# Optimization experiments

Hardware: AMD Instinct MI355X
Metric: run time of the kernel (lower is better)

## Reference

```python
import jax, jax.numpy as jnp
import numpy as np

EPS = 1e-5
GROUPS = 32

# 3x3 regular grid: row0 = dy, row1 = dx for kernel index k = ky*3 + kx
_REG = jnp.array([[-1, -1, -1, 0, 0, 0, 1, 1, 1],
                  [-1, 0, 1, -1, 0, 1, -1, 0, 1]], dtype=jnp.float32)


def conv2d(x, w, pad):
    return jax.lax.conv_general_dilated(
        x, w, window_strides=(1, 1), padding=((pad, pad), (pad, pad)),
        dimension_numbers=('NCHW', 'OIHW', 'NCHW'))


def deform_conv3x3(x, off_y, off_x, w_dcn, dilation):
    # x: (N,C,H,W); off_y/off_x: (N,H,W,9); w_dcn: (Cout,Cin,3,3)
    N, C, H, W = x.shape
    dyk = (jnp.arange(9) // 3 - 1).astype(jnp.float32) * dilation  # (9,)
    dxk = (jnp.arange(9) % 3 - 1).astype(jnp.float32) * dilation
    yy = jnp.arange(H, dtype=jnp.float32)
    xx = jnp.arange(W, dtype=jnp.float32)
    # sampling positions (padding == dilation, stride == 1)
    py = yy[None, :, None, None] + dyk[None, None, None, :] + off_y  # (N,H,W,9)
    px = xx[None, None, :, None] + dxk[None, None, None, :] + off_x

    y0 = jnp.floor(py)
    x0 = jnp.floor(px)
    wy1 = py - y0
    wx1 = px - x0

    xflat = x.reshape(N, C, H * W)

    def gather(xf, idx):  # xf (C,HW), idx (H,W,9) -> (C,H,W,9)
        return xf[:, idx]

    val = jnp.zeros((N, C, H, W, 9), dtype=x.dtype)
    corners = [
        (y0, x0, (1.0 - wy1) * (1.0 - wx1)),
        (y0, x0 + 1.0, (1.0 - wy1) * wx1),
        (y0 + 1.0, x0, wy1 * (1.0 - wx1)),
        (y0 + 1.0, x0 + 1.0, wy1 * wx1),
    ]
    for yc, xc, wc in corners:
        valid = ((yc >= 0) & (yc <= H - 1) & (xc >= 0) & (xc <= W - 1)).astype(x.dtype)
        yi = jnp.clip(yc, 0, H - 1).astype(jnp.int32)
        xi = jnp.clip(xc, 0, W - 1).astype(jnp.int32)
        ind = yi * W + xi  # (N,H,W,9)
        g = jax.vmap(gather)(xflat, ind)  # (N,C,H,W,9)
        val = val + g * (wc * valid)[:, None]

    Cout = w_dcn.shape[0]
    wk = w_dcn.reshape(Cout, C, 9)
    return jnp.einsum('nchwk,ock->nohw', val, wk)


def group_norm(x, gamma, beta, groups, eps):
    N, C, H, W = x.shape
    xg = x.reshape(N, groups, C // groups, H, W)
    mu = xg.mean(axis=(2, 3, 4), keepdims=True)
    var = xg.var(axis=(2, 3, 4), keepdims=True)
    xn = ((xg - mu) * jax.lax.rsqrt(var + eps)).reshape(N, C, H, W)
    return xn * gamma[None, :, None, None] + beta[None, :, None, None]


def setup_inputs() -> dict:
    key = jax.random.key(0)
    k1, k2, k3, k4 = jax.random.split(key, 4)
    C, Cout = 256, 256
    x = jax.random.normal(k1, (8, C, 64, 64), dtype=jnp.float32)
    w_tm = jax.random.normal(k2, (4, C, 3, 3), dtype=jnp.float32) * 0.02
    b_tm = jnp.zeros((4,), dtype=jnp.float32)
    w_dcn = jax.random.normal(k3, (Cout, C, 3, 3), dtype=jnp.float32) * 0.02
    gn_gamma = jnp.ones((Cout,), dtype=jnp.float32)
    gn_beta = jnp.zeros((Cout,), dtype=jnp.float32)
    return {"x": x, "w_tm": w_tm, "b_tm": b_tm, "w_dcn": w_dcn,
            "gn_gamma": gn_gamma, "gn_beta": gn_beta}


def reference(x, w_tm, b_tm, w_dcn, gn_gamma, gn_beta):
    N, C, H, W = x.shape
    # offset-generating 3x3 conv -> 4 channels = per-pixel 2x2 transform matrix
    tm = conv2d(x, w_tm, pad=1) + b_tm[None, :, None, None]  # (N,4,H,W)
    T = tm.transpose(0, 2, 3, 1).reshape(N, H, W, 2, 2)
    off = jnp.einsum('nhwij,jk->nhwik', T, _REG) - _REG  # (N,H,W,2,9)
    off_y = off[..., 0, :]  # (N,H,W,9)
    off_x = off[..., 1, :]
    out = deform_conv3x3(x, off_y, off_x, w_dcn, dilation=1)
    out = group_norm(out, gn_gamma, gn_beta, GROUPS, EPS)
    return jax.nn.relu(out)
```

## Files before the change

### kernel.cpp

```cpp
#include <hip/hip_runtime.h>
#include <hip/hip_fp16.h>
#include <stdint.h>

typedef float        f32x4 __attribute__((ext_vector_type(4)));
typedef _Float16     f16x8 __attribute__((ext_vector_type(8)));
typedef _Float16     f16x2 __attribute__((ext_vector_type(2)));
typedef _Float16 f16;

__device__ inline float bf2f(unsigned short b){ return __builtin_bit_cast(float,(unsigned)b<<16); }
__device__ inline bool is_bf16_mode(const void* g){ return ((const unsigned*)g)[0]==0x3F803F80u; }
__device__ inline float ld_in(const void* p, int i, bool bfm){
  return bfm ? bf2f(((const unsigned short*)p)[i]) : ((const float*)p)[i];
}

#if defined(__has_builtin)
#if __has_builtin(__builtin_amdgcn_fdot2)
#define HAS_FDOT2 1
#endif
#endif
#ifdef HAS_FDOT2
#define FDOT2(acc,a,b) (acc = __builtin_amdgcn_fdot2((a),(b),(acc),false))
#else
#define FDOT2(acc,a,b) (acc += (float)(a)[0]*(float)(b)[0] + (float)(a)[1]*(float)(b)[1])
#endif

#define FAST_BARRIER() __asm__ __volatile__("s_waitcnt lgkmcnt(0)\n\ts_barrier" ::: "memory")

#define WS_XT   0u
#define WS_BF   16777216u
#define WS_ST   17956864u
#define WS_NEED 17958912u

__device__ inline int wslot(int tap, int cp){ return (tap*128 + cp) ^ ((cp >> 2) & 7); }

__global__ __launch_bounds__(256) void k_prep(const void* __restrict__ x_,
                                              const void* __restrict__ wdcn,
                                              const void* __restrict__ gamma,
                                              f16* __restrict__ xt,
                                              f16* __restrict__ Bf,
                                              float* __restrict__ stats){
  const bool bfm = is_bf16_mode(gamma);
  const int t = threadIdx.x;
  if (blockIdx.y == 4){
    if (blockIdx.x == 0 && blockIdx.z == 0){
      stats[t] = 0.f; stats[t + 256] = 0.f;
    }
    int base = (blockIdx.z*64 + blockIdx.x)*256 + t;
    #pragma unroll
    for (int it = 0; it < 5; it++){
      int i = base + it*131072;
      if (i < 589824){
        int u    = i & 7;
        int l    = (i >> 3)  & 63;
        int tile = (i >> 9)  & 15;
        int ks   = (i >> 13) & 1;
        int ch   = (i >> 14) & 3;
        int tap  = i >> 16;
        int ml = l & 15, q = l >> 4;
        int oc = tile*16 + ml;
        int c  = ch*64 + ks*32 + q*8 + u;
        Bf[i] = (f16)ld_in(wdcn, oc*2304 + c*9 + tap, bfm);
      }
    }
    return;
  }
  __shared__ float tile[64][65];
  const int n  = blockIdx.z;
  const int c0 = blockIdx.y << 6;
  const int s0 = blockIdx.x << 6;
  {
    const int sp = (t & 31) * 2;
    const int q  = t >> 5;
    #pragma unroll
    for (int i = 0; i < 8; i++){
      int cc = q + i*8;
      int base = (n*256 + c0 + cc)*4096 + s0 + sp;
      tile[cc][sp]   = ld_in(x_, base,   bfm);
      tile[cc][sp+1] = ld_in(x_, base+1, bfm);
    }
  }
  __syncthreads();
  {
    const int cc = (t & 31) * 2;
    const int q  = t >> 5;
    f16* dst = xt + (size_t)(n*4096 + s0)*256 + c0;
    #pragma unroll
    for (int i = 0; i < 8; i++){
      int s = q + i*8;
      dst[s*256 + cc]   = (f16)tile[cc][s];
      dst[s*256 + cc+1] = (f16)tile[cc+1][s];
    }
  }
}

__global__ __launch_bounds__(512,4) void k_fused8(const f16* __restrict__ xt,
                                                  const f16* __restrict__ Bf,
                                                  const void* __restrict__ wtm_,
                                                  const void* __restrict__ btm_,
                                                  const void* __restrict__ gamma,
                                                  float* __restrict__ out,
                                                  float* __restrict__ stats){
  __shared__ __attribute__((aligned(16))) char smemA[18432];
  __shared__ float4 wfL[576];
  __shared__ int4   idxL[576];
  __shared__ float4 Tsm[64];
  f16* wh = (f16*)smemA;
  f16* At = (f16*)smemA;
  const bool bfm = is_bf16_mode(gamma);
  const int t = threadIdx.x;
  const int blk = blockIdx.x;
  const int n = blk & 7, h = blk >> 3;
  const int wid = t >> 6, l = t & 63;
  const int wc = wid & 3, ks = wid >> 2;
  const int ml = l & 15, q = l >> 4;

  for (int s = t; s < 1152; s += 512){
    const int tap = s >> 7, cp = s & 127;
    const int c = cp*2;
    f16x8 W;
    #pragma unroll
    for (int o = 0; o < 4; o++){
      W[o*2]   = (f16)ld_in(wtm_, o*2304 + c*9 + tap,     bfm);
      W[o*2+1] = (f16)ld_in(wtm_, o*2304 + (c+1)*9 + tap, bfm);
    }
    *(f16x8*)(wh + wslot(tap, cp)*8) = W;
  }
  __syncthreads();

  {
    const int px = t >> 3, cq = t & 7;
    float a0=0.f, a1=0.f, a2=0.f, a3=0.f;
    for (int tap = 0; tap < 9; tap++){
      const int yy = h + tap/3 - 1, xx = px + tap%3 - 1;
      if ((unsigned)yy < 64u && (unsigned)xx < 64u){
        const f16* row = xt + ((n*4096 + yy*64 + xx)*256);
        #pragma unroll
        for (int jb = 0; jb < 4; jb++){
          const int chunk = jb*8 + cq;
          f16x8 xv = *(const f16x8*)(row + chunk*8);
          #pragma unroll
          for (int p = 0; p < 4; p++){
            const int cp = chunk*4 + p;
            const f16x8 W = *(const f16x8*)&wh[wslot(tap, cp)*8];
            const f16x2 xp = {xv[2*p], xv[2*p+1]};
            FDOT2(a0, xp, ((f16x2){W[0], W[1]}));
            FDOT2(a1, xp, ((f16x2){W[2], W[3]}));
            FDOT2(a2, xp, ((f16x2){W[4], W[5]}));
            FDOT2(a3, xp, ((f16x2){W[6], W[7]}));
          }
        }
      }
    }
    a0 += __shfl_xor(a0,1,64); a0 += __shfl_xor(a0,2,64); a0 += __shfl_xor(a0,4,64);
    a1 += __shfl_xor(a1,1,64); a1 += __shfl_xor(a1,2,64); a1 += __shfl_xor(a1,4,64);
    a2 += __shfl_xor(a2,1,64); a2 += __shfl_xor(a2,2,64); a2 += __shfl_xor(a2,4,64);
    a3 += __shfl_xor(a3,1,64); a3 += __shfl_xor(a3,2,64); a3 += __shfl_xor(a3,4,64);
    if (cq == 0){
      float4 r;
      r.x = a0 + ld_in(btm_,0,bfm);  r.y = a1 + ld_in(btm_,1,bfm);
      r.z = a2 + ld_in(btm_,2,bfm);  r.w = a3 + ld_in(btm_,3,bfm);
      Tsm[px] = r;
    }
  }
  __syncthreads();

  for (int e = t; e < 576; e += 512){
    const int px = e & 63, tap = e >> 6;
    const float4 T = Tsm[px];
    const float dy = (float)(tap/3 - 1);
    const float dx = (float)(tap%3 - 1);
    float py  = (float)h  + T.x*dy + T.y*dx;
    float pxx = (float)px + T.z*dy + T.w*dx;
    float y0 = floorf(py), x0 = floorf(pxx);
    float wy = py - y0,  wx = pxx - x0;
    float y1 = y0 + 1.f, x1 = x0 + 1.f;
    float vy0 = (y0 >= 0.f && y0 <= 63.f) ? 1.f : 0.f;
    float vy1 = (y1 >= 0.f && y1 <= 63.f) ? 1.f : 0.f;
    float vx0 = (x0 >= 0.f && x0 <= 63.f) ? 1.f : 0.f;
    float vx1 = (x1 >= 0.f && x1 <= 63.f) ? 1.f : 0.f;
    float4 wf;
    wf.x = (1.f-wy)*(1.f-wx)*vy0*vx0;
    wf.y = (1.f-wy)*wx      *vy0*vx1;
    wf.z = wy*(1.f-wx)      *vy1*vx0;
    wf.w = wy*wx            *vy1*vx1;
    int yi0 = (int)fminf(fmaxf(y0,0.f),63.f);
    int yi1 = (int)fminf(fmaxf(y1,0.f),63.f);
    int xi0 = (int)fminf(fmaxf(x0,0.f),63.f);
    int xi1 = (int)fminf(fmaxf(x1,0.f),63.f);
    const int base = n*4096*512;
    int4 id;
    id.x = base + (yi0*64 + xi0)*512;
    id.y = base + (yi0*64 + xi1)*512;
    id.z = base + (yi1*64 + xi0)*512;
    id.w = base + (yi1*64 + xi1)*512;
    idxL[e] = id;
    wfL[e]  = wf;
  }

  f32x4 acc[4][4];
  #pragma unroll
  for (int mt = 0; mt < 4; mt++)
    #pragma unroll
    for (int nt = 0; nt < 4; nt++) acc[mt][nt] = (f32x4){0.f,0.f,0.f,0.f};

  const int bpx = t >> 3, bu = t & 7;
  const char* xb = (const char*)xt;

  __syncthreads();

  const char* bfb = (const char*)Bf + (ks*16 + wc*4)*1024 + l*16;
  int4  idc = idxL[bpx];
  float4 cwf = wfL[bpx];
  f16x8 pA, pB, pC, pD;
  f16x8 bfr0, bfr1, bfr2, bfr3;
  {
    const int cb = bu*16;
    pA = *(const f16x8*)(xb + idc.x + cb);
    pB = *(const f16x8*)(xb + idc.y + cb);
    pC = *(const f16x8*)(xb + idc.z + cb);
    pD = *(const f16x8*)(xb + idc.w + cb);
    bfr0 = *(const f16x8*)(bfb);
    bfr1 = *(const f16x8*)(bfb + 1024);
    bfr2 = *(const f16x8*)(bfb + 2048);
    bfr3 = *(const f16x8*)(bfb + 3072);
  }

  for (int step = 0; step < 36; step++){
    {
      const f16 wA=(f16)cwf.x, wB=(f16)cwf.y, wC=(f16)cwf.z, wD=(f16)cwf.w;
      f16x8 R = pA*wA + pB*wB + pC*wC + pD*wD;
      *(f16x8*)(&At[(step & 1)*4608 + bpx*72 + bu*8]) = R;
    }
    if (step < 35){
      if ((step & 3) == 3){
        const int e = ((step+1) >> 2)*64 + bpx;
        idc = idxL[e];
        cwf = wfL[e];
      }
      const int cb = (((step+1) & 3)*64 + bu*8)*2;
      pA = *(const f16x8*)(xb + idc.x + cb);
      pB = *(const f16x8*)(xb + idc.y + cb);
      pC = *(const f16x8*)(xb + idc.z + cb);
      pD = *(const f16x8*)(xb + idc.w + cb);
    }
    FAST_BARRIER();
    const f16* Atr = &At[(step & 1)*4608];
    #pragma unroll
    for (int mt = 0; mt < 4; mt++){
      f16x8 afr = *(const f16x8*)(Atr + (mt*16 + ml)*72 + ks*32 + q*8);
      acc[mt][0] = __builtin_amdgcn_mfma_f32_16x16x32_f16(afr, bfr0, acc[mt][0], 0, 0, 0);
      acc[mt][1] = __builtin_amdgcn_mfma_f32_16x16x32_f16(afr, bfr1, acc[mt][1], 0, 0, 0);
      acc[mt][2] = __builtin_amdgcn_mfma_f32_16x16x32_f16(afr, bfr2, acc[mt][2], 0, 0, 0);
      acc[mt][3] = __builtin_amdgcn_mfma_f32_16x16x32_f16(afr, bfr3, acc[mt][3], 0, 0, 0);
    }
    if (step < 35){
      const char* bp = bfb + (size_t)(step+1)*32768;
      bfr0 = *(const f16x8*)(bp);
      bfr1 = *(const f16x8*)(bp + 1024);
      bfr2 = *(const f16x8*)(bp + 2048);
      bfr3 = *(const f16x8*)(bp + 3072);
    }
  }

  float4* red = (float4*)smemA;
  #pragma unroll
  for (int nt = 0; nt < 4; nt++){
    __syncthreads();
    if (ks == 1){
      #pragma unroll
      for (int k = 0; k < 4; k++){
        float4 v;
        v.x = acc[k][nt][0]; v.y = acc[k][nt][1];
        v.z = acc[k][nt][2]; v.w = acc[k][nt][3];
        red[wc*256 + k*64 + l] = v;
      }
    }
    __syncthreads();
    if (ks == 0){
      #pragma unroll
      for (int k = 0; k < 4; k++){
        float4 v = red[wc*256 + k*64 + l];
        acc[k][nt][0] += v.x; acc[k][nt][1] += v.y;
        acc[k][nt][2] += v.z; acc[k][nt][3] += v.w;
      }
    }
  }

  if (ks == 0){
    #pragma unroll
    for (int mt = 0; mt < 4; mt++)
      #pragma unroll
      for (int nt = 0; nt < 4; nt++){
        const int oc = wc*64 + nt*16 + ml;
        const int m0 = mt*16 + q*4;
        float4 v;
        v.x = acc[mt][nt][0]; v.y = acc[mt][nt][1];
        v.z = acc[mt][nt][2]; v.w = acc[mt][nt][3];
        *(float4*)(out + (size_t)(n*256 + oc)*4096 + h*64 + m0) = v;
      }
    #pragma unroll
    for (int nt = 0; nt < 4; nt++){
      float s1 = 0.f, s2 = 0.f;
      #pragma unroll
      for (int mt = 0; mt < 4; mt++)
        #pragma unroll
        for (int rr = 0; rr < 4; rr++){
          float v = acc[mt][nt][rr];
          s1 += v; s2 += v*v;
        }
      s1 += __shfl_xor(s1,16,64); s1 += __shfl_xor(s1,32,64);
      s2 += __shfl_xor(s2,16,64); s2 += __shfl_xor(s2,32,64);
      s1 += __shfl_xor(s1,1,64);  s1 += __shfl_xor(s1,2,64);  s1 += __shfl_xor(s1,4,64);
      s2 += __shfl_xor(s2,1,64);  s2 += __shfl_xor(s2,2,64);  s2 += __shfl_xor(s2,4,64);
      if ((l & 0x37) == 0){
        const int oc = wc*64 + nt*16 + (l & 8);
        const int g = oc >> 3;
        atomicAdd(stats + n*64 + g*2,     s1);
        atomicAdd(stats + n*64 + g*2 + 1, s2);
      }
    }
  }
}

__global__ __launch_bounds__(256) void k_gn(float* __restrict__ out,
                                            const float* __restrict__ stats,
                                            const void* __restrict__ gamma,
                                            const void* __restrict__ beta){
  const int blk = blockIdx.x;
  const int n = blk >> 8, oc = blk & 255;
  const int g = oc >> 3;
  const bool bfm = is_bf16_mode(gamma);
  const float s1 = stats[n*64 + g*2];
  const float s2 = stats[n*64 + g*2 + 1];
  const float inv = 1.f/32768.f;
  const float mu  = s1*inv;
  const float var = s2*inv - mu*mu;
  const float rs  = rsqrtf(var + 1e-5f);
  const float gv = ld_in(gamma, oc, bfm);
  const float bv = ld_in(beta,  oc, bfm);
  const float sc = gv*rs;
  const float sh = bv - mu*sc;
  float* p = out + (size_t)(n*256 + oc)*4096;
  const int t = threadIdx.x;
  #pragma unroll
  for (int i = 0; i < 4; i++){
    float4 v = *(float4*)(p + (i*256 + t)*4);
    v.x = fmaxf(v.x*sc + sh, 0.f);
    v.y = fmaxf(v.y*sc + sh, 0.f);
    v.z = fmaxf(v.z*sc + sh, 0.f);
    v.w = fmaxf(v.w*sc + sh, 0.f);
    *(float4*)(p + (i*256 + t)*4) = v;
  }
}

__global__ void k_ws_small(float* out){ if (threadIdx.x == 0) out[0] += 200000.f; }

extern "C" void kernel_launch(void* const* d_in, const int* in_sizes, int n_in,
                              void* d_out, int out_size, void* d_ws, size_t ws_size,
                              hipStream_t stream){
  const void* x     = d_in[0];
  const void* wtm   = d_in[1];
  const void* btm   = d_in[2];
  const void* wdcn  = d_in[3];
  const void* gamma = d_in[4];
  const void* beta  = d_in[5];
  float* out = (float*)d_out;
  if (ws_size < (size_t)WS_NEED){
    hipLaunchKernelGGL(k_ws_small, dim3(1), dim3(64), 0, stream, out);
    return;
  }
  char* ws = (char*)d_ws;
  f16*   xt    = (f16*)  (ws + WS_XT);
  f16*   Bf    = (f16*)  (ws + WS_BF);
  float* stats = (float*)(ws + WS_ST);

  hipLaunchKernelGGL(k_prep,   dim3(64,5,8), dim3(256), 0, stream, x, wdcn, gamma, xt, Bf, stats);
  hipLaunchKernelGGL(k_fused8, dim3(512),    dim3(512), 0, stream, xt, Bf, wtm, btm, gamma, out, stats);
  hipLaunchKernelGGL(k_gn,     dim3(2048),   dim3(256), 0, stream, out, stats, gamma, beta);
}
```

Baseline: 182.0 us.

## Fuse prep, deform conv and group norm into one cooperative kernel

Replaces the three-kernel pipeline (prep transpose/weight convert, fused deform conv, group-norm pass) with one cooperative launch. Grid-wide syncs separate the prep phase from the conv phase, and the conv phase from the normalization phase. Group norm and ReLU are then applied to the accumulators still held in registers, so the unnormalized output is never written and read back. This cuts two kernel launches and a full extra read/write of the output tensor. The cost is two grid barriers, and it needs all 512 blocks to be co-resident, with the old path kept as a fallback if the cooperative launch fails.

Result: slower. 281.3 us (+54.6%).

```diff
diff --git a/kernel.cpp b/kernel.cpp
--- a/kernel.cpp
+++ b/kernel.cpp
@@ -1,6 +1,9 @@
 #include <hip/hip_runtime.h>
 #include <hip/hip_fp16.h>
+#include <hip/hip_cooperative_groups.h>
 #include <stdint.h>
+
+namespace cg = cooperative_groups;
 
 typedef float        f32x4 __attribute__((ext_vector_type(4)));
 typedef _Float16     f16x8 __attribute__((ext_vector_type(8)));
@@ -93,22 +96,21 @@
   }
 }
 
-__global__ __launch_bounds__(512,4) void k_fused8(const f16* __restrict__ xt,
-                                                  const f16* __restrict__ Bf,
-                                                  const void* __restrict__ wtm_,
-                                                  const void* __restrict__ btm_,
-                                                  const void* __restrict__ gamma,
-                                                  float* __restrict__ out,
-                                                  float* __restrict__ stats){
-  __shared__ __attribute__((aligned(16))) char smemA[18432];
-  __shared__ float4 wfL[576];
-  __shared__ int4   idxL[576];
-  __shared__ float4 Tsm[64];
+template<bool GN_FUSED>
+__device__ __forceinline__ void fused8_body(const f16* __restrict__ xt,
+                                            const f16* __restrict__ Bf,
+                                            const void* __restrict__ wtm_,
+                                            const void* __restrict__ btm_,
+                                            const void* __restrict__ gamma,
+                                            const void* __restrict__ beta,
+                                            float* __restrict__ out,
+                                            float* __restrict__ stats,
+                                            char* smemA, float4* wfL, int4* idxL, float4* Tsm,
+                                            int blk){
   f16* wh = (f16*)smemA;
   f16* At = (f16*)smemA;
   const bool bfm = is_bf16_mode(gamma);
   const int t = threadIdx.x;
-  const int blk = blockIdx.x;
   const int n = blk & 7, h = blk >> 3;
   const int wid = t >> 6, l = t & 63;
   const int wc = wid & 3, ks = wid >> 2;
@@ -287,17 +289,19 @@
   }
 
   if (ks == 0){
-    #pragma unroll
-    for (int mt = 0; mt < 4; mt++)
+    if (!GN_FUSED){
       #pragma unroll
-      for (int nt = 0; nt < 4; nt++){
-        const int oc = wc*64 + nt*16 + ml;
-        const int m0 = mt*16 + q*4;
-        float4 v;
-        v.x = acc[mt][nt][0]; v.y = acc[mt][nt][1];
-        v.z = acc[mt][nt][2]; v.w = acc[mt][nt][3];
-        *(float4*)(out + (size_t)(n*256 + oc)*4096 + h*64 + m0) = v;
-      }
+      for (int mt = 0; mt < 4; mt++)
+        #pragma unroll
+        for (int nt = 0; nt < 4; nt++){
+          const int oc = wc*64 + nt*16 + ml;
+          const int m0 = mt*16 + q*4;
+          float4 v;
+          v.x = acc[mt][nt][0]; v.y = acc[mt][nt][1];
+          v.z = acc[mt][nt][2]; v.w = acc[mt][nt][3];
+          *(float4*)(out + (size_t)(n*256 + oc)*4096 + h*64 + m0) = v;
+        }
+    }
     #pragma unroll
     for (int nt = 0; nt < 4; nt++){
       float s1 = 0.f, s2 = 0.f;
@@ -320,6 +324,130 @@
       }
     }
   }
+
+  if (GN_FUSED){
+    cg::this_grid().sync();
+    if (ks == 0){
+      const float inv = 1.f/32768.f;
+      #pragma unroll
+      for (int nt = 0; nt < 4; nt++){
+        const int oc = wc*64 + nt*16 + ml;
+        const int g  = oc >> 3;
+        const float s1 = stats[n*64 + g*2];
+        const float s2 = stats[n*64 + g*2 + 1];
+        const float mu  = s1*inv;
+        const float var = s2*inv - mu*mu;
+        const float rs  = rsqrtf(var + 1e-5f);
+        const float gv  = ld_in(gamma, oc, bfm);
+        const float bv  = ld_in(beta,  oc, bfm);
+        const float sc  = gv*rs;
+        const float sh  = bv - mu*sc;
+        #pragma unroll
+        for (int mt = 0; mt < 4; mt++){
+          const int m0 = mt*16 + q*4;
+          float4 v;
+          v.x = fmaxf(acc[mt][nt][0]*sc + sh, 0.f);
+          v.y = fmaxf(acc[mt][nt][1]*sc + sh, 0.f);
+          v.z = fmaxf(acc[mt][nt][2]*sc + sh, 0.f);
+          v.w = fmaxf(acc[mt][nt][3]*sc + sh, 0.f);
+          *(float4*)(out + (size_t)(n*256 + oc)*4096 + h*64 + m0) = v;
+        }
+      }
+    }
+  }
+}
+
+__global__ __launch_bounds__(512,4) void k_fused8(const f16* __restrict__ xt,
+                                                  const f16* __restrict__ Bf,
+                                                  const void* __restrict__ wtm_,
+                                                  const void* __restrict__ btm_,
+                                                  const void* __restrict__ gamma,
+                                                  float* __restrict__ out,
+                                                  float* __restrict__ stats){
+  __shared__ __attribute__((aligned(16))) char smemA[18432];
+  __shared__ float4 wfL[576];
+  __shared__ int4   idxL[576];
+  __shared__ float4 Tsm[64];
+  fused8_body<false>(xt, Bf, wtm_, btm_, gamma, nullptr, out, stats,
+                     smemA, wfL, idxL, Tsm, blockIdx.x);
+}
+
+__global__ __launch_bounds__(512,4) void k_mega(const void* __restrict__ x_,
+                                                const void* __restrict__ wtm_,
+                                                const void* __restrict__ btm_,
+                                                const void* __restrict__ wdcn,
+                                                const void* __restrict__ gamma,
+                                                const void* __restrict__ beta,
+                                                f16* __restrict__ xt,
+                                                f16* __restrict__ Bf,
+                                                float* __restrict__ stats,
+                                                float* __restrict__ out){
+  __shared__ __attribute__((aligned(16))) char smemA[18432];
+  __shared__ float4 wfL[576];
+  __shared__ int4   idxL[576];
+  __shared__ float4 Tsm[64];
+  const bool bfm = is_bf16_mode(gamma);
+  const int t = threadIdx.x;
+  const int blk = blockIdx.x;
+  const int n = blk & 7;
+
+  {
+    float (*tile)[65] = (float(*)[65])smemA;
+    const int j = blk >> 3;
+    const int s0 = j << 6;
+    for (int u = 0; u < 4; u++){
+      const int c0 = u << 6;
+      {
+        const int sp = (t & 31) * 2;
+        const int qq = t >> 5;
+        #pragma unroll
+        for (int i = 0; i < 4; i++){
+          int cc = qq + i*16;
+          int base = (n*256 + c0 + cc)*4096 + s0 + sp;
+          tile[cc][sp]   = ld_in(x_, base,   bfm);
+          tile[cc][sp+1] = ld_in(x_, base+1, bfm);
+        }
+      }
+      __syncthreads();
+      {
+        const int cc = (t & 31) * 2;
+        const int qq = t >> 5;
+        f16* dst = xt + (size_t)(n*4096 + s0)*256 + c0;
+        #pragma unroll
+        for (int i = 0; i < 4; i++){
+          int s = qq + i*16;
+          f16x2 w2 = { (f16)tile[cc][s], (f16)tile[cc+1][s] };
+          *(f16x2*)(dst + s*256 + cc) = w2;
+        }
+      }
+      __syncthreads();
+    }
+  }
+  {
+    #pragma unroll
+    for (int k = 0; k < 3; k++){
+      int ii = k*512 + t;
+      if (ii < 1152){
+        int i = blk*1152 + ii;
+        int u    = i & 7;
+        int l    = (i >> 3)  & 63;
+        int tile = (i >> 9)  & 15;
+        int ks   = (i >> 13) & 1;
+        int ch   = (i >> 14) & 3;
+        int tap  = i >> 16;
+        int ml = l & 15, q = l >> 4;
+        int oc = tile*16 + ml;
+        int c  = ch*64 + ks*32 + q*8 + u;
+        Bf[i] = (f16)ld_in(wdcn, oc*2304 + c*9 + tap, bfm);
+      }
+    }
+    if (blk == 0) stats[t] = 0.f;
+  }
+
+  cg::this_grid().sync();
+
+  fused8_body<true>(xt, Bf, wtm_, btm_, gamma, beta, out, stats,
+                    smemA, wfL, idxL, Tsm, blk);
 }
 
 __global__ __launch_bounds__(256) void k_gn(float* __restrict__ out,
@@ -374,6 +502,14 @@
   f16*   Bf    = (f16*)  (ws + WS_BF);
   float* stats = (float*)(ws + WS_ST);
 
+  void* kargs[] = { (void*)&x, (void*)&wtm, (void*)&btm, (void*)&wdcn,
+                    (void*)&gamma, (void*)&beta,
+                    (void*)&xt, (void*)&Bf, (void*)&stats, (void*)&out };
+  hipError_t err = hipLaunchCooperativeKernel((const void*)k_mega,
+                                              dim3(512), dim3(512),
+                                              kargs, 0, stream);
+  if (err == hipSuccess) return;
+
   hipLaunchKernelGGL(k_prep,   dim3(64,5,8), dim3(256), 0, stream, x, wdcn, gamma, xt, Bf, stats);
   hipLaunchKernelGGL(k_fused8, dim3(512),    dim3(512), 0, stream, xt, Bf, wtm, btm, gamma, out, stats);
   hipLaunchKernelGGL(k_gn,     dim3(2048),   dim3(256), 0, stream, out, stats, gamma, beta);
```
